# Performance work log

Measured on AMD Instinct MI355X. Metric: run time of the kernel, lower is better.

The kernel has to match this reference:

```python
import jax, jax.numpy as jnp
import numpy as np

K_NEIGHBORS = 16
BN_EPS = 1e-5


def _bn(h, g, b):
    # train-mode BatchNorm1d over (batch, points) per channel, biased variance
    mu = h.mean(axis=(0, 1))
    var = h.var(axis=(0, 1))
    return g * (h - mu) * jax.lax.rsqrt(var + BN_EPS) + b


def _gather(arr, idx):
    # arr: [B,N,D], idx: [B,N,K] -> [B,N,K,D]
    return jax.vmap(lambda a, i: a[i])(arr, idx)


def setup_inputs() -> dict:
    key = jax.random.key(0)
    ks = jax.random.split(key, 16)
    B, N, Cin, C, H, M = 4, 4096, 64, 64, 32, 4
    rn = lambda k, s: jax.random.normal(k, s, dtype=jnp.float32) * 0.05
    return {
        "x": jax.random.normal(ks[0], (B, N, Cin), dtype=jnp.float32),
        "p": jax.random.normal(ks[1], (B, N, 3), dtype=jnp.float32),
        "fc1_w": rn(ks[2], (Cin, C)), "fc1_b": jnp.zeros((C,), jnp.float32),
        "bn1_g": jnp.ones((C,), jnp.float32), "bn1_b": jnp.zeros((C,), jnp.float32),
        "qkv_w": rn(ks[3], (C, 3 * C)),
        "pos_w1": rn(ks[4], (3, H)), "pos_b1": jnp.zeros((H,), jnp.float32),
        "pos_w2": rn(ks[5], (H, C)), "pos_b2": jnp.zeros((C,), jnp.float32),
        "attn_w1": rn(ks[6], (C, M * C)), "attn_b1": jnp.zeros((M * C,), jnp.float32),
        "attn_w2": rn(ks[7], (M * C, C)), "attn_b2": jnp.zeros((C,), jnp.float32),
        "bn2_g": jnp.ones((C,), jnp.float32), "bn2_b": jnp.zeros((C,), jnp.float32),
        "fc2_w": rn(ks[8], (C, C)), "fc2_b": jnp.zeros((C,), jnp.float32),
        "bn3_g": jnp.ones((C,), jnp.float32), "bn3_b": jnp.zeros((C,), jnp.float32),
    }


def reference(x, p, fc1_w, fc1_b, bn1_g, bn1_b, qkv_w,
              pos_w1, pos_b1, pos_w2, pos_b2,
              attn_w1, attn_b1, attn_w2, attn_b2,
              bn2_g, bn2_b, fc2_w, fc2_b, bn3_g, bn3_b):
    C = fc1_w.shape[1]
    # fc1 -> BN -> ReLU
    h = jax.nn.relu(_bn(x @ fc1_w + fc1_b, bn1_g, bn1_b))
    residual = h

    # PointTransformerLayer (vector attention over kNN; mask is all-ones)
    qkv = h @ qkv_w  # [B,N,3C]
    q, k, v = qkv[..., :C], qkv[..., C:2 * C], qkv[..., 2 * C:]
    # squared pairwise distances (matches norm-based topk ranking)
    sq = jnp.sum(p * p, axis=-1)  # [B,N]
    d2 = sq[:, :, None] + sq[:, None, :] - 2.0 * jnp.einsum('bnd,bmd->bnm', p, p)
    _, idx = jax.lax.top_k(-d2, K_NEIGHBORS)  # k smallest distances, [B,N,K]

    kj = _gather(k, idx)          # [B,N,K,C]
    vj = _gather(v, idx)          # [B,N,K,C]
    pj = _gather(p, idx)          # [B,N,K,3]

    rel_pos = p[:, :, None, :] - pj                      # [B,N,K,3]
    pe = jax.nn.relu(rel_pos @ pos_w1 + pos_b1) @ pos_w2 + pos_b2  # [B,N,K,C]

    qk_rel = q[:, :, None, :] - kj                       # [B,N,K,C]
    vv = vj + pe
    sim = jax.nn.relu((qk_rel + pe) @ attn_w1 + attn_b1) @ attn_w2 + attn_b2
    attn = jax.nn.softmax(sim, axis=2)                   # softmax over neighbors
    agg = jnp.sum(attn * vv, axis=2)                     # [B,N,C]

    h2 = jax.nn.relu(_bn(agg, bn2_g, bn2_b))
    y = jax.nn.relu(_bn((h2 + residual) @ fc2_w + fc2_b, bn3_g, bn3_b))
    return (y, p)
```

## Files before the change

kernel.cpp:

```cpp
#include <hip/hip_runtime.h>
#include <math.h>

constexpr int kB = 4, kN = 4096, kK = 16;
constexpr int kRows = kB * kN;
constexpr float kEps = 1e-5f;
constexpr float kFltMax = 3.402823466e38f;
constexpr int kCap = 240;

typedef __attribute__((ext_vector_type(8))) short short8;
typedef __attribute__((ext_vector_type(4))) float f32x4;

__device__ __forceinline__ unsigned short f2bf(float x) {
  return (unsigned short)((__float_as_uint(x) + 0x8000u) >> 16);
}
__device__ __forceinline__ unsigned int pkbf(float lo, float hi) {
  return ((__float_as_uint(lo) + 0x8000u) >> 16) |
         ((__float_as_uint(hi) + 0x8000u) & 0xffff0000u);
}
__device__ __forceinline__ short8 pack8f(float4 a, float4 b) {
  union { unsigned int u[4]; short8 s; } pk;
  pk.u[0] = pkbf(a.x, a.y);
  pk.u[1] = pkbf(a.z, a.w);
  pk.u[2] = pkbf(b.x, b.y);
  pk.u[3] = pkbf(b.z, b.w);
  return pk.s;
}

__device__ __forceinline__ int lane_prefix(unsigned long long m) {
  return __builtin_amdgcn_mbcnt_hi((unsigned)(m >> 32),
         __builtin_amdgcn_mbcnt_lo((unsigned)m, 0));
}

__device__ __forceinline__ void bitonic64(float& sv, int& si, int lane) {
  #pragma unroll
  for (int k = 2; k <= 64; k <<= 1) {
    #pragma unroll
    for (int j = k >> 1; j > 0; j >>= 1) {
      float ov = __shfl_xor(sv, j);
      int   oi = __shfl_xor(si, j);
      bool up = ((lane & k) == 0);
      bool lower = ((lane & j) == 0);
      bool osm = (ov < sv) || (ov == sv && oi < si);
      bool take = (lower == up) ? osm : !osm;
      if (take) { sv = ov; si = oi; }
    }
  }
}

__global__ __launch_bounds__(256) void fc1_conv_kernel(
    const float* __restrict__ x, const float* __restrict__ w,
    const float* __restrict__ bias,
    const float* __restrict__ aw1, const float* __restrict__ aw2,
    const float* __restrict__ pw2, const float* __restrict__ qw,
    const float* __restrict__ f2w,
    const float* __restrict__ pin, float* __restrict__ p4o,
    unsigned short* __restrict__ wpak,
    float* __restrict__ out) {
  __shared__ unsigned short wf[8 * 512];
  const int t = threadIdx.x;
  const int blk = blockIdx.x;
  {
    int id = blk * 256 + t;
    if (id < 16384) {
      int j = id & 7, lane = (id >> 3) & 63, rest = id >> 9;
      int mt = rest >> 1, hh = rest & 1;
      wpak[id] = f2bf(aw1[(32 * hh + 8 * (lane >> 4) + j) * 256 + mt * 16 + (lane & 15)]);
      float3 pp = *reinterpret_cast<const float3*>(pin + 3 * id);
      float4 o;
      o.x = pp.x; o.y = pp.y; o.z = pp.z;
      o.w = pp.x * pp.x + pp.y * pp.y + pp.z * pp.z;
      *reinterpret_cast<float4*>(p4o + 4 * id) = o;
    } else if (id < 32768) {
      int i = id - 16384;
      int j = i & 7, lane = (i >> 3) & 63, rest = i >> 9;
      int ct = rest >> 3, f = rest & 7;
      wpak[id] = f2bf(aw2[(32 * f + 8 * (lane >> 4) + j) * 64 + ct * 16 + (lane & 15)]);
    } else if (id < 34816) {
      int i = id - 32768;
      int c = i >> 5, hh = i & 31;
      wpak[id] = f2bf(pw2[hh * 64 + c]);
    } else if (id < 47104) {
      int i = id - 34816;
      int j = i & 7, lane = (i >> 3) & 63, rest = i >> 9;
      int ct = rest >> 1, hh = rest & 1;
      wpak[id] = f2bf(qw[(32 * hh + 8 * (lane >> 4) + j) * 192 + ct * 16 + (lane & 15)]);
    } else if (id < 51200) {
      int i = id - 47104;
      int j = i & 7, lane = (i >> 3) & 63, rest = i >> 9;
      int ct = rest >> 1, hh = rest & 1;
      wpak[id] = f2bf(f2w[(32 * hh + 8 * (lane >> 4) + j) * 64 + ct * 16 + (lane & 15)]);
    }
  }
  for (int i = t; i < 4096; i += 256) {
    int j = i & 7, lane = (i >> 3) & 63, rest = i >> 9;
    int ct = rest >> 1, hh = rest & 1;
    wf[i] = f2bf(w[(32 * hh + 8 * (lane >> 4) + j) * 64 + ct * 16 + (lane & 15)]);
  }
  __syncthreads();
  const int lane = t & 63, wv = t >> 6;
  const int l = lane & 15, q = lane >> 4;
  const int r0 = blk * 64;
  const int row = r0 + wv * 16 + l;
  const f32x4 zero = {0.f, 0.f, 0.f, 0.f};
  float4 xa0 = *reinterpret_cast<const float4*>(&x[row * 64 + q * 8]);
  float4 xa1 = *reinterpret_cast<const float4*>(&x[row * 64 + q * 8 + 4]);
  float4 xb0 = *reinterpret_cast<const float4*>(&x[row * 64 + 32 + q * 8]);
  float4 xb1 = *reinterpret_cast<const float4*>(&x[row * 64 + 32 + q * 8 + 4]);
  short8 a0 = pack8f(xa0, xa1), a1 = pack8f(xb0, xb1);
  #pragma unroll
  for (int ct = 0; ct < 4; ++ct) {
    short8 b0 = *reinterpret_cast<const short8*>(&wf[(ct * 2 + 0) * 512 + lane * 8]);
    short8 b1 = *reinterpret_cast<const short8*>(&wf[(ct * 2 + 1) * 512 + lane * 8]);
    f32x4 acc = __builtin_amdgcn_mfma_f32_16x16x32_bf16(a0, b0, zero, 0, 0, 0);
    acc = __builtin_amdgcn_mfma_f32_16x16x32_bf16(a1, b1, acc, 0, 0, 0);
    const float bc = bias[ct * 16 + l];
    #pragma unroll
    for (int i = 0; i < 4; ++i)
      out[(r0 + wv * 16 + q * 4 + i) * 64 + ct * 16 + l] = acc[i] + bc;
  }
}

__global__ void stats_part_kernel(const float* __restrict__ src, float* __restrict__ part) {
  __shared__ float sb[256], sb2[256];
  const int t = threadIdx.x, blk = blockIdx.x;
  const int c = t & 63, rg = t >> 6;
  float s = 0.f, s2 = 0.f;
  for (int r = rg; r < 64; r += 4) {
    float v = src[(blk * 64 + r) * 64 + c];
    s += v; s2 += v * v;
  }
  sb[t] = s; sb2[t] = s2; __syncthreads();
  if (t < 64) {
    float ts  = sb[t] + sb[64 + t] + sb[128 + t] + sb[192 + t];
    float ts2 = sb2[t] + sb2[64 + t] + sb2[128 + t] + sb2[192 + t];
    part[blk * 128 + t] = ts;
    part[blk * 128 + 64 + t] = ts2;
  }
}

__global__ void stats_fin_kernel(const float* __restrict__ part,
                                 const float* __restrict__ g, const float* __restrict__ b,
                                 float* __restrict__ A, float* __restrict__ Bv) {
  const int c = threadIdx.x;
  double s = 0.0, s2 = 0.0;
  for (int i = 0; i < 256; ++i) { s += part[i * 128 + c]; s2 += part[i * 128 + 64 + c]; }
  double mean = s / (double)kRows;
  double var = s2 / (double)kRows - mean * mean;
  float rs = (float)(1.0 / sqrt(var + (double)kEps));
  float Af = g[c] * rs;
  A[c] = Af;
  Bv[c] = b[c] - (float)mean * Af;
}

__global__ __launch_bounds__(256) void qkv_bn_kernel(
    const float* __restrict__ hpre, const float* __restrict__ A1,
    const float* __restrict__ B1, const unsigned short* __restrict__ wqf,
    float* __restrict__ hout, unsigned short* __restrict__ out) {
  const int t = threadIdx.x, lane = t & 63, wv = t >> 6;
  const int l = lane & 15, q = lane >> 4;
  const int r0 = blockIdx.x * 64;
  const int row = r0 + wv * 16 + l;
  const f32x4 zero = {0.f, 0.f, 0.f, 0.f};
  short8 af[2];
  #pragma unroll
  for (int hh = 0; hh < 2; ++hh) {
    const int c0 = 32 * hh + q * 8;
    float4 v0 = *reinterpret_cast<const float4*>(&hpre[row * 64 + c0]);
    float4 v1 = *reinterpret_cast<const float4*>(&hpre[row * 64 + c0 + 4]);
    float4 Aa = *reinterpret_cast<const float4*>(&A1[c0]);
    float4 Ab = *reinterpret_cast<const float4*>(&A1[c0 + 4]);
    float4 Ba = *reinterpret_cast<const float4*>(&B1[c0]);
    float4 Bb = *reinterpret_cast<const float4*>(&B1[c0 + 4]);
    v0.x = fmaxf(Aa.x * v0.x + Ba.x, 0.f); v0.y = fmaxf(Aa.y * v0.y + Ba.y, 0.f);
    v0.z = fmaxf(Aa.z * v0.z + Ba.z, 0.f); v0.w = fmaxf(Aa.w * v0.w + Ba.w, 0.f);
    v1.x = fmaxf(Ab.x * v1.x + Bb.x, 0.f); v1.y = fmaxf(Ab.y * v1.y + Bb.y, 0.f);
    v1.z = fmaxf(Ab.z * v1.z + Bb.z, 0.f); v1.w = fmaxf(Ab.w * v1.w + Bb.w, 0.f);
    *reinterpret_cast<float4*>(&hout[row * 64 + c0]) = v0;
    *reinterpret_cast<float4*>(&hout[row * 64 + c0 + 4]) = v1;
    af[hh] = pack8f(v0, v1);
  }
  #pragma unroll
  for (int ct = 0; ct < 12; ++ct) {
    short8 b0 = *reinterpret_cast<const short8*>(&wqf[((ct * 2 + 0) * 64 + lane) * 8]);
    short8 b1 = *reinterpret_cast<const short8*>(&wqf[((ct * 2 + 1) * 64 + lane) * 8]);
    f32x4 acc = __builtin_amdgcn_mfma_f32_16x16x32_bf16(af[0], b0, zero, 0, 0, 0);
    acc = __builtin_amdgcn_mfma_f32_16x16x32_bf16(af[1], b1, acc, 0, 0, 0);
    #pragma unroll
    for (int i = 0; i < 4; ++i)
      out[(r0 + wv * 16 + q * 4 + i) * 192 + ct * 16 + l] = f2bf(acc[i]);
  }
}

__global__ __launch_bounds__(256) void knn_attn_kernel(
    const float* __restrict__ p4, const unsigned short* __restrict__ qkv,
    const float* __restrict__ pos_w1, const float* __restrict__ pos_b1,
    const float* __restrict__ pos_b2,
    const float* __restrict__ attn_b1, const float* __restrict__ attn_b2,
    const unsigned short* __restrict__ w1f,
    const unsigned short* __restrict__ w2f,
    const unsigned short* __restrict__ pw2t,
    float* __restrict__ agg) {
  __shared__ unsigned short Ulds[64 * 72];
  __shared__ float VVlds[64 * 68];
  __shared__ int   scnt[4];
  __shared__ float sthr[4];

  const int t = threadIdx.x;
  const int lane = t & 63, w = t >> 6;
  const int l = lane & 15, q = lane >> 4;
  const int work = ((blockIdx.x & 7) << 9) | (blockIdx.x >> 3);
  const int b = work >> 10;
  const int pt_row = work * 4 + w;
  const int qrow0 = work * 4;
  const int base = b * kN;
  const f32x4 zero = {0.f, 0.f, 0.f, 0.f};

  if (t < 4) scnt[t] = 0;

  const float4 q0f = *reinterpret_cast<const float4*>(p4 + 4 * (qrow0 + 0));
  const float4 q1f = *reinterpret_cast<const float4*>(p4 + 4 * (qrow0 + 1));
  const float4 q2f = *reinterpret_cast<const float4*>(p4 + 4 * (qrow0 + 2));
  const float4 q3f = *reinterpret_cast<const float4*>(p4 + 4 * (qrow0 + 3));
  const float4 qp4 = *reinterpret_cast<const float4*>(p4 + 4 * pt_row);
  const float qx = qp4.x, qy = qp4.y, qz = qp4.z, sqq = qp4.w;

  auto d2q = [](const float4& Q, const float4& C) -> float {
    float dt = fmaf(Q.z, C.z, fmaf(Q.y, C.y, Q.x * C.x));
    return fmaf(-2.0f, dt, Q.w + C.w);
  };
  unsigned pk0[8], pk1[8], pk2[8], pk3[8];
  float lmin = kFltMax;
  const int cbase = base + w * 1024;
  #pragma unroll
  for (int g = 0; g < 2; ++g) {
    float4 cc[8];
    #pragma unroll
    for (int jj = 0; jj < 8; ++jj)
      cc[jj] = *reinterpret_cast<const float4*>(p4 + 4 * (cbase + (g * 8 + jj) * 64 + lane));
    #pragma unroll
    for (int jj = 0; jj < 8; ++jj) {
      float dot = fmaf(qz, cc[jj].z, fmaf(qy, cc[jj].y, qx * cc[jj].x));
      lmin = fminf(lmin, fmaf(-2.0f, dot, sqq + cc[jj].w));
    }
    #pragma unroll
    for (int pi = 0; pi < 4; ++pi) {
      const float4 ca = cc[2 * pi], cb = cc[2 * pi + 1];
      pk0[g * 4 + pi] = (__float_as_uint(d2q(q0f, ca)) >> 16) |
                        (__float_as_uint(d2q(q0f, cb)) & 0xffff0000u);
      pk1[g * 4 + pi] = (__float_as_uint(d2q(q1f, ca)) >> 16) |
                        (__float_as_uint(d2q(q1f, cb)) & 0xffff0000u);
      pk2[g * 4 + pi] = (__float_as_uint(d2q(q2f, ca)) >> 16) |
                        (__float_as_uint(d2q(q2f, cb)) & 0xffff0000u);
      pk3[g * 4 + pi] = (__float_as_uint(d2q(q3f, ca)) >> 16) |
                        (__float_as_uint(d2q(q3f, cb)) & 0xffff0000u);
    }
  }
  {
    int dummy = lane;
    float lm = lmin;
    bitonic64(lm, dummy, lane);
    float s16 = __shfl(lm, 15);
    if (lane == 0) sthr[w] = s16 + 1e-3f;
  }
  __syncthreads();

  {
    auto append_q = [&](const unsigned (&PK)[8], int j) {
      int* listj = reinterpret_cast<int*>(VVlds + j * 1088);
      const float thrj = sthr[j];
      #pragma unroll
      for (int g = 0; g < 2; ++g) {
        unsigned long long m[8];
        int pc[8];
        #pragma unroll
        for (int c = 0; c < 8; ++c) {
          unsigned pku = PK[g * 4 + (c >> 1)];
          float dv = (c & 1) ? __uint_as_float(pku & 0xffff0000u)
                             : __uint_as_float(pku << 16);
          m[c] = __ballot(dv <= thrj);
          pc[c] = __popcll(m[c]);
        }
        int tot = pc[0] + pc[1] + pc[2] + pc[3] + pc[4] + pc[5] + pc[6] + pc[7];
        int old = 0;
        if (lane == 0) old = atomicAdd(&scnt[j], tot);
        old = __shfl(old, 0);
        int pre = 0;
        #pragma unroll
        for (int c = 0; c < 8; ++c) {
          if ((m[c] >> lane) & 1ull) {
            int pos = old + pre + lane_prefix(m[c]);
            if (pos < kCap) listj[pos] = w * 1024 + (g * 8 + c) * 64 + lane;
          }
          pre += pc[c];
        }
      }
    };
    append_q(pk0, 0);
    append_q(pk1, 1);
    append_q(pk2, 2);
    append_q(pk3, 3);
  }
  __syncthreads();

  const int n = scnt[w];
  int* bufi = reinterpret_cast<int*>(VVlds + w * 1088);
  float sv = kFltMax;
  int   si = 0x7fffffff;
  if (n <= kCap) {
    for (int g0 = 0; g0 < n; g0 += 48) {
      float mv; int mi;
      if (lane < 16) { mv = sv; mi = si; }
      else {
        int pos = g0 + (lane - 16);
        if (pos < n) {
          int jj = bufi[pos];
          float4 c = *reinterpret_cast<const float4*>(p4 + 4 * (base + jj));
          float dot = fmaf(qz, c.z, fmaf(qy, c.y, qx * c.x));
          mv = fmaf(-2.0f, dot, sqq + c.w);
          mi = jj;
        } else { mv = kFltMax; mi = 0x7fffffff; }
      }
      bitonic64(mv, mi, lane);
      sv = mv; si = mi;
    }
  } else {
    for (int g0 = 0; g0 < kN; g0 += 48) {
      float mv; int mi;
      if (lane < 16) { mv = sv; mi = si; }
      else {
        int j = g0 + (lane - 16);
        if (j < kN) {
          float4 c = *reinterpret_cast<const float4*>(p4 + 4 * (base + j));
          float dot = fmaf(qz, c.z, fmaf(qy, c.y, qx * c.x));
          mv = fmaf(-2.0f, dot, sqq + c.w);
          mi = j;
        } else { mv = kFltMax; mi = 0x7fffffff; }
      }
      bitonic64(mv, mi, lane);
      sv = mv; si = mi;
    }
  }

  int idxv = 0;
  if (lane < 16) {
    int o = si;
    if ((unsigned)o >= (unsigned)kN) o = 0;
    idxv = o;
  }

  asm volatile("" ::: "memory");

  {
    const int r = lane >> 2, seg = lane & 3;
    const unsigned short* jrow = qkv + (base + __shfl(idxv, r)) * 192;
    const int c0 = seg * 16;
    uint4 k0 = *reinterpret_cast<const uint4*>(jrow + 64 + c0);
    uint4 k1 = *reinterpret_cast<const uint4*>(jrow + 64 + c0 + 8);
    uint4 v0 = *reinterpret_cast<const uint4*>(jrow + 128 + c0);
    uint4 v1 = *reinterpret_cast<const uint4*>(jrow + 128 + c0 + 8);
    uint4 q0 = *reinterpret_cast<const uint4*>(qkv + pt_row * 192 + c0);
    uint4 q1 = *reinterpret_cast<const uint4*>(qkv + pt_row * 192 + c0 + 8);
    auto diff2 = [](unsigned int qu, unsigned int ku) -> unsigned int {
      float lo = __uint_as_float(qu << 16) - __uint_as_float(ku << 16);
      float hi = __uint_as_float(qu & 0xffff0000u) - __uint_as_float(ku & 0xffff0000u);
      return pkbf(lo, hi);
    };
    uint4 u0, u1;
    u0.x = diff2(q0.x, k0.x); u0.y = diff2(q0.y, k0.y);
    u0.z = diff2(q0.z, k0.z); u0.w = diff2(q0.w, k0.w);
    u1.x = diff2(q1.x, k1.x); u1.y = diff2(q1.y, k1.y);
    u1.z = diff2(q1.z, k1.z); u1.w = diff2(q1.w, k1.w);
    *reinterpret_cast<uint4*>(&Ulds[(w * 16 + r) * 72 + c0]) = u0;
    *reinterpret_cast<uint4*>(&Ulds[(w * 16 + r) * 72 + c0 + 8]) = u1;
    const unsigned int vs[8] = {v0.x, v0.y, v0.z, v0.w, v1.x, v1.y, v1.z, v1.w};
    #pragma unroll
    for (int i = 0; i < 4; ++i) {
      float4 vv;
      vv.x = __uint_as_float(vs[2 * i] << 16);
      vv.y = __uint_as_float(vs[2 * i] & 0xffff0000u);
      vv.z = __uint_as_float(vs[2 * i + 1] << 16);
      vv.w = __uint_as_float(vs[2 * i + 1] & 0xffff0000u);
      *reinterpret_cast<float4*>(&VVlds[(w * 16 + r) * 68 + c0 + 4 * i]) = vv;
    }
  }
  short8 pbf;
  {
    const int nj = __shfl(idxv, l);
    const float4 pj4 = *reinterpret_cast<const float4*>(p4 + 4 * (base + nj));
    float rx = qx - pj4.x, ry = qy - pj4.y, rz = qz - pj4.z;
    float hv[8];
    #pragma unroll
    for (int j = 0; j < 8; ++j) {
      int hh = q * 8 + j;
      hv[j] = fmaxf(pos_b1[hh] + rx * pos_w1[hh] + ry * pos_w1[32 + hh] +
                    rz * pos_w1[64 + hh], 0.0f);
    }
    union { unsigned int u[4]; short8 s; } pk;
    #pragma unroll
    for (int ii = 0; ii < 4; ++ii) pk.u[ii] = pkbf(hv[2 * ii], hv[2 * ii + 1]);
    pbf = pk.s;
  }

  {
    const int urow = (w * 16 + l) * 72;
    const int vrow = (w * 16 + l) * 68;
    #pragma unroll
    for (int mt = 0; mt < 4; ++mt) {
      short8 paf = *reinterpret_cast<const short8*>(&pw2t[(mt * 16 + l) * 32 + q * 8]);
      f32x4 pe = __builtin_amdgcn_mfma_f32_16x16x32_bf16(paf, pbf, zero, 0, 0, 0);
      const int c0 = mt * 16 + q * 4;
      float4 b2v = *reinterpret_cast<const float4*>(&pos_b2[c0]);
      float pe0 = pe[0] + b2v.x, pe1 = pe[1] + b2v.y;
      float pe2 = pe[2] + b2v.z, pe3 = pe[3] + b2v.w;
      uint2 u2 = *reinterpret_cast<uint2*>(&Ulds[urow + c0]);
      uint2 o;
      o.x = pkbf(__uint_as_float(u2.x << 16) + pe0,
                 __uint_as_float(u2.x & 0xffff0000u) + pe1);
      o.y = pkbf(__uint_as_float(u2.y << 16) + pe2,
                 __uint_as_float(u2.y & 0xffff0000u) + pe3);
      *reinterpret_cast<uint2*>(&Ulds[urow + c0]) = o;
      float4 vv = *reinterpret_cast<float4*>(&VVlds[vrow + c0]);
      vv.x += pe0; vv.y += pe1; vv.z += pe2; vv.w += pe3;
      *reinterpret_cast<float4*>(&VVlds[vrow + c0]) = vv;
    }
  }

  unsigned int plo[16], phi[16];
  {
    const int urow = (w * 16 + l) * 72;
    short8 ub0 = *reinterpret_cast<const short8*>(&Ulds[urow + q * 8]);
    short8 ub1 = *reinterpret_cast<const short8*>(&Ulds[urow + 32 + q * 8]);
    #pragma unroll
    for (int mt = 0; mt < 16; ++mt) {
      short8 a0 = *reinterpret_cast<const short8*>(&w1f[(mt * 2 + 0) * 512 + lane * 8]);
      short8 a1 = *reinterpret_cast<const short8*>(&w1f[(mt * 2 + 1) * 512 + lane * 8]);
      f32x4 acc = __builtin_amdgcn_mfma_f32_16x16x32_bf16(a0, ub0, zero, 0, 0, 0);
      acc = __builtin_amdgcn_mfma_f32_16x16x32_bf16(a1, ub1, acc, 0, 0, 0);
      float4 bb = *reinterpret_cast<const float4*>(&attn_b1[mt * 16 + q * 4]);
      plo[mt] = pkbf(fmaxf(acc[0] + bb.x, 0.f), fmaxf(acc[1] + bb.y, 0.f));
      phi[mt] = pkbf(fmaxf(acc[2] + bb.z, 0.f), fmaxf(acc[3] + bb.w, 0.f));
    }
  }

  {
    f32x4 acc2[4];
    #pragma unroll
    for (int ct = 0; ct < 4; ++ct) acc2[ct] = zero;
    const int sbase = l + 32 * (q & 1);
    const bool hi_mt = (q >= 2);
    #pragma unroll
    for (int f = 0; f < 8; ++f) {
      union { unsigned int u[4]; short8 s; } pk;
      #pragma unroll
      for (int d = 0; d < 4; ++d) {
        const int src = sbase + ((d >> 1) << 4);
        const unsigned int w0 = (d & 1) ? phi[2 * f] : plo[2 * f];
        const unsigned int w1v = (d & 1) ? phi[2 * f + 1] : plo[2 * f + 1];
        unsigned int va = (unsigned int)__shfl((int)w0, src);
        unsigned int vb = (unsigned int)__shfl((int)w1v, src);
        pk.u[d] = hi_mt ? vb : va;
      }
      short8 afr = pk.s;
      #pragma unroll
      for (int ct = 0; ct < 4; ++ct) {
        short8 bfr = *reinterpret_cast<const short8*>(&w2f[((ct * 8 + f) * 64 + lane) * 8]);
        acc2[ct] = __builtin_amdgcn_mfma_f32_16x16x32_bf16(afr, bfr, acc2[ct], 0, 0, 0);
      }
    }
    #pragma unroll
    for (int ct = 0; ct < 4; ++ct) {
      const int ch = ct * 16 + l;
      const float bv = attn_b2[ch];
      float s0v = acc2[ct][0] + bv, s1v = acc2[ct][1] + bv;
      float s2v = acc2[ct][2] + bv, s3v = acc2[ct][3] + bv;
      float mx = fmaxf(fmaxf(s0v, s1v), fmaxf(s2v, s3v));
      mx = fmaxf(mx, __shfl_xor(mx, 16, 64));
      mx = fmaxf(mx, __shfl_xor(mx, 32, 64));
      float e0 = __expf(s0v - mx), e1 = __expf(s1v - mx);
      float e2 = __expf(s2v - mx), e3 = __expf(s3v - mx);
      float se = e0 + e1 + e2 + e3;
      se += __shfl_xor(se, 16, 64);
      se += __shfl_xor(se, 32, 64);
      const int vbase = (w * 16 + q * 4) * 68 + ch;
      float a = e0 * VVlds[vbase] + e1 * VVlds[vbase + 68] +
                e2 * VVlds[vbase + 136] + e3 * VVlds[vbase + 204];
      a += __shfl_xor(a, 16, 64);
      a += __shfl_xor(a, 32, 64);
      if (q == 0) agg[pt_row * 64 + ch] = a / se;
    }
  }
}

__global__ __launch_bounds__(256) void fc2_mfma_kernel(
    const float* __restrict__ aggp, const float* __restrict__ hres,
    const float* __restrict__ A2, const float* __restrict__ B2,
    const unsigned short* __restrict__ fc2f, const float* __restrict__ bias,
    float* __restrict__ z) {
  const int t = threadIdx.x, lane = t & 63, wv = t >> 6;
  const int l = lane & 15, q = lane >> 4;
  const int r0 = blockIdx.x * 64;
  const int row = r0 + wv * 16 + l;
  const f32x4 zero = {0.f, 0.f, 0.f, 0.f};
  short8 af[2];
  #pragma unroll
  for (int hh = 0; hh < 2; ++hh) {
    const int c0 = 32 * hh + q * 8;
    float4 v0 = *reinterpret_cast<const float4*>(&aggp[row * 64 + c0]);
    float4 v1 = *reinterpret_cast<const float4*>(&aggp[row * 64 + c0 + 4]);
    float4 r0v = *reinterpret_cast<const float4*>(&hres[row * 64 + c0]);
    float4 r1v = *reinterpret_cast<const float4*>(&hres[row * 64 + c0 + 4]);
    float4 Aa = *reinterpret_cast<const float4*>(&A2[c0]);
    float4 Ab = *reinterpret_cast<const float4*>(&A2[c0 + 4]);
    float4 Ba = *reinterpret_cast<const float4*>(&B2[c0]);
    float4 Bb = *reinterpret_cast<const float4*>(&B2[c0 + 4]);
    v0.x = fmaxf(Aa.x * v0.x + Ba.x, 0.f) + r0v.x;
    v0.y = fmaxf(Aa.y * v0.y + Ba.y, 0.f) + r0v.y;
    v0.z = fmaxf(Aa.z * v0.z + Ba.z, 0.f) + r0v.z;
    v0.w = fmaxf(Aa.w * v0.w + Ba.w, 0.f) + r0v.w;
    v1.x = fmaxf(Ab.x * v1.x + Bb.x, 0.f) + r1v.x;
    v1.y = fmaxf(Ab.y * v1.y + Bb.y, 0.f) + r1v.y;
    v1.z = fmaxf(Ab.z * v1.z + Bb.z, 0.f) + r1v.z;
    v1.w = fmaxf(Ab.w * v1.w + Bb.w, 0.f) + r1v.w;
    af[hh] = pack8f(v0, v1);
  }
  #pragma unroll
  for (int ct = 0; ct < 4; ++ct) {
    short8 b0 = *reinterpret_cast<const short8*>(&fc2f[((ct * 2 + 0) * 64 + lane) * 8]);
    short8 b1 = *reinterpret_cast<const short8*>(&fc2f[((ct * 2 + 1) * 64 + lane) * 8]);
    f32x4 acc = __builtin_amdgcn_mfma_f32_16x16x32_bf16(af[0], b0, zero, 0, 0, 0);
    acc = __builtin_amdgcn_mfma_f32_16x16x32_bf16(af[1], b1, acc, 0, 0, 0);
    const float bc = bias[ct * 16 + l];
    #pragma unroll
    for (int i = 0; i < 4; ++i)
      z[(r0 + wv * 16 + q * 4 + i) * 64 + ct * 16 + l] = acc[i] + bc;
  }
}

__global__ void final_kernel(const float* __restrict__ z, const float* __restrict__ A3,
                             const float* __restrict__ B3, const float* __restrict__ p,
                             float* __restrict__ y) {
  const int blk = blockIdx.x, t = threadIdx.x;
  if (blk < 4096) {
    int i = blk * 256 + t;
    int c = i & 63;
    y[i] = fmaxf(A3[c] * z[i] + B3[c], 0.0f);
  } else {
    int i = (blk - 4096) * 256 + t;
    y[1048576 + i] = p[i];
  }
}

extern "C" void kernel_launch(void* const* d_in, const int* in_sizes, int n_in,
                              void* d_out, int out_size, void* d_ws, size_t ws_size,
                              hipStream_t stream) {
  const float* x       = (const float*)d_in[0];
  const float* p       = (const float*)d_in[1];
  const float* fc1_w   = (const float*)d_in[2];
  const float* fc1_b   = (const float*)d_in[3];
  const float* bn1_g   = (const float*)d_in[4];
  const float* bn1_b   = (const float*)d_in[5];
  const float* qkv_w   = (const float*)d_in[6];
  const float* pos_w1  = (const float*)d_in[7];
  const float* pos_b1  = (const float*)d_in[8];
  const float* pos_w2  = (const float*)d_in[9];
  const float* pos_b2  = (const float*)d_in[10];
  const float* attn_w1 = (const float*)d_in[11];
  const float* attn_b1 = (const float*)d_in[12];
  const float* attn_w2 = (const float*)d_in[13];
  const float* attn_b2 = (const float*)d_in[14];
  const float* bn2_g   = (const float*)d_in[15];
  const float* bn2_b   = (const float*)d_in[16];
  const float* fc2_w   = (const float*)d_in[17];
  const float* fc2_b   = (const float*)d_in[18];
  const float* bn3_g   = (const float*)d_in[19];
  const float* bn3_b   = (const float*)d_in[20];

  float* ws   = (float*)d_ws;
  float* h    = ws;
  unsigned short* qkvb = (unsigned short*)(ws + 1048576);
  float* hpre = ws + 4194304;
  float* aggv = ws + 5242880;
  float* z    = ws + 6291456;
  float* st   = ws + 7340032;
  float* p4   = ws + 7356800;
  unsigned short* wpak = (unsigned short*)(ws + 7618944);
  unsigned short* w1f  = wpak;
  unsigned short* w2f  = wpak + 16384;
  unsigned short* pw2t = wpak + 32768;
  unsigned short* wqf  = wpak + 34816;
  unsigned short* fc2f = wpak + 47104;

  float* A1 = st,       *B1 = st + 64;
  float* A2 = st + 128, *B2 = st + 192;
  float* A3 = st + 256, *B3 = st + 320;
  float* y = (float*)d_out;

  fc1_conv_kernel<<<256, 256, 0, stream>>>(x, fc1_w, fc1_b, attn_w1, attn_w2,
                                           pos_w2, qkv_w, fc2_w, p, p4, wpak, hpre);
  stats_part_kernel<<<256, 256, 0, stream>>>(hpre, aggv);
  stats_fin_kernel<<<1, 64, 0, stream>>>(aggv, bn1_g, bn1_b, A1, B1);
  qkv_bn_kernel<<<256, 256, 0, stream>>>(hpre, A1, B1, wqf, h, qkvb);
  knn_attn_kernel<<<4096, 256, 0, stream>>>(p4, qkvb, pos_w1, pos_b1, pos_b2,
                                            attn_b1, attn_b2, w1f, w2f, pw2t, aggv);
  stats_part_kernel<<<256, 256, 0, stream>>>(aggv, z);
  stats_fin_kernel<<<1, 64, 0, stream>>>(z, bn2_g, bn2_b, A2, B2);
  fc2_mfma_kernel<<<256, 256, 0, stream>>>(aggv, h, A2, B2, fc2f, fc2_b, z);
  stats_part_kernel<<<256, 256, 0, stream>>>(z, aggv);
  stats_fin_kernel<<<1, 64, 0, stream>>>(aggv, bn3_g, bn3_b, A3, B3);
  final_kernel<<<4288, 256, 0, stream>>>(z, A3, B3, p, y);
}
```

Before: 288.4 us.

## Tighten kNN candidate threshold across waves, store VV in bf16, interleave MLP layers

```diff
diff --git a/kernel.cpp b/kernel.cpp
--- a/kernel.cpp
+++ b/kernel.cpp
@@ -16,6 +16,11 @@
 __device__ __forceinline__ unsigned int pkbf(float lo, float hi) {
   return ((__float_as_uint(lo) + 0x8000u) >> 16) |
          ((__float_as_uint(hi) + 0x8000u) & 0xffff0000u);
+}
+__device__ __forceinline__ float bflo(unsigned int u) { return __uint_as_float(u << 16); }
+__device__ __forceinline__ float bfhi(unsigned int u) { return __uint_as_float(u & 0xffff0000u); }
+__device__ __forceinline__ float bfu16(unsigned short us) {
+  return __uint_as_float(((unsigned int)us) << 16);
 }
 __device__ __forceinline__ short8 pack8f(float4 a, float4 b) {
   union { unsigned int u[4]; short8 s; } pk;
@@ -45,6 +50,11 @@
       if (take) { sv = ov; si = oi; }
     }
   }
+}
+
+__device__ __forceinline__ float d2q(const float4& Q, const float4& C) {
+  float dt = fmaf(Q.z, C.z, fmaf(Q.y, C.y, Q.x * C.x));
+  return fmaf(-2.0f, dt, Q.w + C.w);
 }
 
 __global__ __launch_bounds__(256) void fc1_conv_kernel(
@@ -201,9 +211,9 @@
     const unsigned short* __restrict__ pw2t,
     float* __restrict__ agg) {
   __shared__ unsigned short Ulds[64 * 72];
-  __shared__ float VVlds[64 * 68];
-  __shared__ int   scnt[4];
-  __shared__ float sthr[4];
+  __shared__ unsigned short VVb[64 * 72];
+  __shared__ float thrs[4];
+  __shared__ int   cnts[4];
 
   const int t = threadIdx.x;
   const int lane = t & 63, w = t >> 6;
@@ -215,21 +225,18 @@
   const int base = b * kN;
   const f32x4 zero = {0.f, 0.f, 0.f, 0.f};
 
-  if (t < 4) scnt[t] = 0;
-
-  const float4 q0f = *reinterpret_cast<const float4*>(p4 + 4 * (qrow0 + 0));
-  const float4 q1f = *reinterpret_cast<const float4*>(p4 + 4 * (qrow0 + 1));
-  const float4 q2f = *reinterpret_cast<const float4*>(p4 + 4 * (qrow0 + 2));
-  const float4 q3f = *reinterpret_cast<const float4*>(p4 + 4 * (qrow0 + 3));
-  const float4 qp4 = *reinterpret_cast<const float4*>(p4 + 4 * pt_row);
-  const float qx = qp4.x, qy = qp4.y, qz = qp4.z, sqq = qp4.w;
-
-  auto d2q = [](const float4& Q, const float4& C) -> float {
-    float dt = fmaf(Q.z, C.z, fmaf(Q.y, C.y, Q.x * C.x));
-    return fmaf(-2.0f, dt, Q.w + C.w);
-  };
-  unsigned pk0[8], pk1[8], pk2[8], pk3[8];
-  float lmin = kFltMax;
+  if (t < 4) cnts[t] = 0;
+
+  float4 qs[4];
+  qs[0] = *reinterpret_cast<const float4*>(p4 + 4 * (qrow0 + 0));
+  qs[1] = *reinterpret_cast<const float4*>(p4 + 4 * (qrow0 + 1));
+  qs[2] = *reinterpret_cast<const float4*>(p4 + 4 * (qrow0 + 2));
+  qs[3] = *reinterpret_cast<const float4*>(p4 + 4 * (qrow0 + 3));
+  const float4 qp4 = (w == 0) ? qs[0] : (w == 1) ? qs[1] : (w == 2) ? qs[2] : qs[3];
+  const float qx = qp4.x, qy = qp4.y, qz = qp4.z;
+
+  unsigned pks[4][8];
+  float lm[4] = {kFltMax, kFltMax, kFltMax, kFltMax};
   const int cbase = base + w * 1024;
   #pragma unroll
   for (int g = 0; g < 2; ++g) {
@@ -238,36 +245,40 @@
     for (int jj = 0; jj < 8; ++jj)
       cc[jj] = *reinterpret_cast<const float4*>(p4 + 4 * (cbase + (g * 8 + jj) * 64 + lane));
     #pragma unroll
-    for (int jj = 0; jj < 8; ++jj) {
-      float dot = fmaf(qz, cc[jj].z, fmaf(qy, cc[jj].y, qx * cc[jj].x));
-      lmin = fminf(lmin, fmaf(-2.0f, dot, sqq + cc[jj].w));
-    }
-    #pragma unroll
     for (int pi = 0; pi < 4; ++pi) {
       const float4 ca = cc[2 * pi], cb = cc[2 * pi + 1];
-      pk0[g * 4 + pi] = (__float_as_uint(d2q(q0f, ca)) >> 16) |
-                        (__float_as_uint(d2q(q0f, cb)) & 0xffff0000u);
-      pk1[g * 4 + pi] = (__float_as_uint(d2q(q1f, ca)) >> 16) |
-                        (__float_as_uint(d2q(q1f, cb)) & 0xffff0000u);
-      pk2[g * 4 + pi] = (__float_as_uint(d2q(q2f, ca)) >> 16) |
-                        (__float_as_uint(d2q(q2f, cb)) & 0xffff0000u);
-      pk3[g * 4 + pi] = (__float_as_uint(d2q(q3f, ca)) >> 16) |
-                        (__float_as_uint(d2q(q3f, cb)) & 0xffff0000u);
-    }
-  }
-  {
+      #pragma unroll
+      for (int j = 0; j < 4; ++j) {
+        float da = d2q(qs[j], ca);
+        float db = d2q(qs[j], cb);
+        lm[j] = fminf(lm[j], fminf(da, db));
+        pks[j][g * 4 + pi] = (__float_as_uint(da) >> 16) |
+                             (__float_as_uint(db) & 0xffff0000u);
+      }
+    }
+  }
+  {
+    float* lmbuf = reinterpret_cast<float*>(Ulds);
+    #pragma unroll
+    for (int j = 0; j < 4; ++j) lmbuf[w * 256 + j * 64 + lane] = lm[j];
+  }
+  __syncthreads();
+
+  {
+    const float* lmbuf = reinterpret_cast<const float*>(Ulds);
+    float cv = fminf(fminf(lmbuf[w * 64 + lane], lmbuf[256 + w * 64 + lane]),
+                     fminf(lmbuf[512 + w * 64 + lane], lmbuf[768 + w * 64 + lane]));
     int dummy = lane;
-    float lm = lmin;
-    bitonic64(lm, dummy, lane);
-    float s16 = __shfl(lm, 15);
-    if (lane == 0) sthr[w] = s16 + 1e-3f;
+    bitonic64(cv, dummy, lane);
+    float s16 = __shfl(cv, 15);
+    if (lane == 0) thrs[w] = s16 + fabsf(s16) * 0.0078125f + 1e-6f;
   }
   __syncthreads();
 
   {
     auto append_q = [&](const unsigned (&PK)[8], int j) {
-      int* listj = reinterpret_cast<int*>(VVlds + j * 1088);
-      const float thrj = sthr[j];
+      int* listj = reinterpret_cast<int*>(VVb + j * 1152);
+      const float thrj = thrs[j];
       #pragma unroll
       for (int g = 0; g < 2; ++g) {
         unsigned long long m[8];
@@ -282,7 +293,7 @@
         }
         int tot = pc[0] + pc[1] + pc[2] + pc[3] + pc[4] + pc[5] + pc[6] + pc[7];
         int old = 0;
-        if (lane == 0) old = atomicAdd(&scnt[j], tot);
+        if (lane == 0) old = atomicAdd(&cnts[j], tot);
         old = __shfl(old, 0);
         int pre = 0;
         #pragma unroll
@@ -295,15 +306,15 @@
         }
       }
     };
-    append_q(pk0, 0);
-    append_q(pk1, 1);
-    append_q(pk2, 2);
-    append_q(pk3, 3);
+    append_q(pks[0], 0);
+    append_q(pks[1], 1);
+    append_q(pks[2], 2);
+    append_q(pks[3], 3);
   }
   __syncthreads();
 
-  const int n = scnt[w];
-  int* bufi = reinterpret_cast<int*>(VVlds + w * 1088);
+  const int n = cnts[w];
+  const int* bufi = reinterpret_cast<const int*>(VVb + w * 1152);
   float sv = kFltMax;
   int   si = 0x7fffffff;
   if (n <= kCap) {
@@ -315,8 +326,7 @@
         if (pos < n) {
           int jj = bufi[pos];
           float4 c = *reinterpret_cast<const float4*>(p4 + 4 * (base + jj));
-          float dot = fmaf(qz, c.z, fmaf(qy, c.y, qx * c.x));
-          mv = fmaf(-2.0f, dot, sqq + c.w);
+          mv = d2q(qp4, c);
           mi = jj;
         } else { mv = kFltMax; mi = 0x7fffffff; }
       }
@@ -331,8 +341,7 @@
         int j = g0 + (lane - 16);
         if (j < kN) {
           float4 c = *reinterpret_cast<const float4*>(p4 + 4 * (base + j));
-          float dot = fmaf(qz, c.z, fmaf(qy, c.y, qx * c.x));
-          mv = fmaf(-2.0f, dot, sqq + c.w);
+          mv = d2q(qp4, c);
           mi = j;
         } else { mv = kFltMax; mi = 0x7fffffff; }
       }
@@ -361,8 +370,8 @@
     uint4 q0 = *reinterpret_cast<const uint4*>(qkv + pt_row * 192 + c0);
     uint4 q1 = *reinterpret_cast<const uint4*>(qkv + pt_row * 192 + c0 + 8);
     auto diff2 = [](unsigned int qu, unsigned int ku) -> unsigned int {
-      float lo = __uint_as_float(qu << 16) - __uint_as_float(ku << 16);
-      float hi = __uint_as_float(qu & 0xffff0000u) - __uint_as_float(ku & 0xffff0000u);
+      float lo = bflo(qu) - bflo(ku);
+      float hi = bfhi(qu) - bfhi(ku);
       return pkbf(lo, hi);
     };
     uint4 u0, u1;
@@ -372,16 +381,8 @@
     u1.z = diff2(q1.z, k1.z); u1.w = diff2(q1.w, k1.w);
     *reinterpret_cast<uint4*>(&Ulds[(w * 16 + r) * 72 + c0]) = u0;
     *reinterpret_cast<uint4*>(&Ulds[(w * 16 + r) * 72 + c0 + 8]) = u1;
-    const unsigned int vs[8] = {v0.x, v0.y, v0.z, v0.w, v1.x, v1.y, v1.z, v1.w};
-    #pragma unroll
-    for (int i = 0; i < 4; ++i) {
-      float4 vv;
-      vv.x = __uint_as_float(vs[2 * i] << 16);
-      vv.y = __uint_as_float(vs[2 * i] & 0xffff0000u);
-      vv.z = __uint_as_float(vs[2 * i + 1] << 16);
-      vv.w = __uint_as_float(vs[2 * i + 1] & 0xffff0000u);
-      *reinterpret_cast<float4*>(&VVlds[(w * 16 + r) * 68 + c0 + 4 * i]) = vv;
-    }
+    *reinterpret_cast<uint4*>(&VVb[(w * 16 + r) * 72 + c0]) = v0;
+    *reinterpret_cast<uint4*>(&VVb[(w * 16 + r) * 72 + c0 + 8]) = v1;
   }
   short8 pbf;
   {
@@ -403,7 +404,6 @@
 
   {
     const int urow = (w * 16 + l) * 72;
-    const int vrow = (w * 16 + l) * 68;
     #pragma unroll
     for (int mt = 0; mt < 4; ++mt) {
       short8 paf = *reinterpret_cast<const short8*>(&pw2t[(mt * 16 + l) * 32 + q * 8]);
@@ -414,48 +414,46 @@
       float pe2 = pe[2] + b2v.z, pe3 = pe[3] + b2v.w;
       uint2 u2 = *reinterpret_cast<uint2*>(&Ulds[urow + c0]);
       uint2 o;
-      o.x = pkbf(__uint_as_float(u2.x << 16) + pe0,
-                 __uint_as_float(u2.x & 0xffff0000u) + pe1);
-      o.y = pkbf(__uint_as_float(u2.y << 16) + pe2,
-                 __uint_as_float(u2.y & 0xffff0000u) + pe3);
+      o.x = pkbf(bflo(u2.x) + pe0, bfhi(u2.x) + pe1);
+      o.y = pkbf(bflo(u2.y) + pe2, bfhi(u2.y) + pe3);
       *reinterpret_cast<uint2*>(&Ulds[urow + c0]) = o;
-      float4 vv = *reinterpret_cast<float4*>(&VVlds[vrow + c0]);
-      vv.x += pe0; vv.y += pe1; vv.z += pe2; vv.w += pe3;
-      *reinterpret_cast<float4*>(&VVlds[vrow + c0]) = vv;
-    }
-  }
-
-  unsigned int plo[16], phi[16];
-  {
+      uint2 v2 = *reinterpret_cast<uint2*>(&VVb[urow + c0]);
+      uint2 ov;
+      ov.x = pkbf(bflo(v2.x) + pe0, bfhi(v2.x) + pe1);
+      ov.y = pkbf(bflo(v2.y) + pe2, bfhi(v2.y) + pe3);
+      *reinterpret_cast<uint2*>(&VVb[urow + c0]) = ov;
+    }
+  }
+
+  {
+    f32x4 acc2[4];
+    #pragma unroll
+    for (int ct = 0; ct < 4; ++ct) acc2[ct] = zero;
     const int urow = (w * 16 + l) * 72;
     short8 ub0 = *reinterpret_cast<const short8*>(&Ulds[urow + q * 8]);
     short8 ub1 = *reinterpret_cast<const short8*>(&Ulds[urow + 32 + q * 8]);
-    #pragma unroll
-    for (int mt = 0; mt < 16; ++mt) {
-      short8 a0 = *reinterpret_cast<const short8*>(&w1f[(mt * 2 + 0) * 512 + lane * 8]);
-      short8 a1 = *reinterpret_cast<const short8*>(&w1f[(mt * 2 + 1) * 512 + lane * 8]);
-      f32x4 acc = __builtin_amdgcn_mfma_f32_16x16x32_bf16(a0, ub0, zero, 0, 0, 0);
-      acc = __builtin_amdgcn_mfma_f32_16x16x32_bf16(a1, ub1, acc, 0, 0, 0);
-      float4 bb = *reinterpret_cast<const float4*>(&attn_b1[mt * 16 + q * 4]);
-      plo[mt] = pkbf(fmaxf(acc[0] + bb.x, 0.f), fmaxf(acc[1] + bb.y, 0.f));
-      phi[mt] = pkbf(fmaxf(acc[2] + bb.z, 0.f), fmaxf(acc[3] + bb.w, 0.f));
-    }
-  }
-
-  {
-    f32x4 acc2[4];
-    #pragma unroll
-    for (int ct = 0; ct < 4; ++ct) acc2[ct] = zero;
     const int sbase = l + 32 * (q & 1);
     const bool hi_mt = (q >= 2);
     #pragma unroll
     for (int f = 0; f < 8; ++f) {
+      unsigned plo2[2], phi2[2];
+      #pragma unroll
+      for (int s = 0; s < 2; ++s) {
+        const int mt = 2 * f + s;
+        short8 a0 = *reinterpret_cast<const short8*>(&w1f[(mt * 2 + 0) * 512 + lane * 8]);
+        short8 a1 = *reinterpret_cast<const short8*>(&w1f[(mt * 2 + 1) * 512 + lane * 8]);
+        f32x4 acc = __builtin_amdgcn_mfma_f32_16x16x32_bf16(a0, ub0, zero, 0, 0, 0);
+        acc = __builtin_amdgcn_mfma_f32_16x16x32_bf16(a1, ub1, acc, 0, 0, 0);
+        float4 bb = *reinterpret_cast<const float4*>(&attn_b1[mt * 16 + q * 4]);
+        plo2[s] = pkbf(fmaxf(acc[0] + bb.x, 0.f), fmaxf(acc[1] + bb.y, 0.f));
+        phi2[s] = pkbf(fmaxf(acc[2] + bb.z, 0.f), fmaxf(acc[3] + bb.w, 0.f));
+      }
       union { unsigned int u[4]; short8 s; } pk;
       #pragma unroll
       for (int d = 0; d < 4; ++d) {
         const int src = sbase + ((d >> 1) << 4);
-        const unsigned int w0 = (d & 1) ? phi[2 * f] : plo[2 * f];
-        const unsigned int w1v = (d & 1) ? phi[2 * f + 1] : plo[2 * f + 1];
+        const unsigned int w0 = (d & 1) ? phi2[0] : plo2[0];
+        const unsigned int w1v = (d & 1) ? phi2[1] : plo2[1];
         unsigned int va = (unsigned int)__shfl((int)w0, src);
         unsigned int vb = (unsigned int)__shfl((int)w1v, src);
         pk.u[d] = hi_mt ? vb : va;
@@ -481,9 +479,9 @@
       float se = e0 + e1 + e2 + e3;
       se += __shfl_xor(se, 16, 64);
       se += __shfl_xor(se, 32, 64);
-      const int vbase = (w * 16 + q * 4) * 68 + ch;
-      float a = e0 * VVlds[vbase] + e1 * VVlds[vbase + 68] +
-                e2 * VVlds[vbase + 136] + e3 * VVlds[vbase + 204];
+      const int vbase = (w * 16 + q * 4) * 72 + ch;
+      float a = e0 * bfu16(VVb[vbase])       + e1 * bfu16(VVb[vbase + 72]) +
+                e2 * bfu16(VVb[vbase + 144]) + e3 * bfu16(VVb[vbase + 216]);
       a += __shfl_xor(a, 16, 64);
       a += __shfl_xor(a, 32, 64);
       if (q == 0) agg[pt_row * 64 + ch] = a / se;
```

Result: slower. 309.5 us (+7.3%).

## Store V+pe in bf16 LDS, interleave attn MLP layers, raise occupancy

Applied to the files above, without the earlier changes.

```diff
diff --git a/kernel.cpp b/kernel.cpp
--- a/kernel.cpp
+++ b/kernel.cpp
@@ -16,6 +16,11 @@
 __device__ __forceinline__ unsigned int pkbf(float lo, float hi) {
   return ((__float_as_uint(lo) + 0x8000u) >> 16) |
          ((__float_as_uint(hi) + 0x8000u) & 0xffff0000u);
+}
+__device__ __forceinline__ float bflo(unsigned int u) { return __uint_as_float(u << 16); }
+__device__ __forceinline__ float bfhi(unsigned int u) { return __uint_as_float(u & 0xffff0000u); }
+__device__ __forceinline__ float bfu16(unsigned short us) {
+  return __uint_as_float(((unsigned int)us) << 16);
 }
 __device__ __forceinline__ short8 pack8f(float4 a, float4 b) {
   union { unsigned int u[4]; short8 s; } pk;
@@ -45,6 +50,11 @@
       if (take) { sv = ov; si = oi; }
     }
   }
+}
+
+__device__ __forceinline__ float d2q(const float4& Q, const float4& C) {
+  float dt = fmaf(Q.z, C.z, fmaf(Q.y, C.y, Q.x * C.x));
+  return fmaf(-2.0f, dt, Q.w + C.w);
 }
 
 __global__ __launch_bounds__(256) void fc1_conv_kernel(
@@ -191,7 +201,7 @@
   }
 }
 
-__global__ __launch_bounds__(256) void knn_attn_kernel(
+__global__ __launch_bounds__(256, 4) void knn_attn_kernel(
     const float* __restrict__ p4, const unsigned short* __restrict__ qkv,
     const float* __restrict__ pos_w1, const float* __restrict__ pos_b1,
     const float* __restrict__ pos_b2,
@@ -201,9 +211,9 @@
     const unsigned short* __restrict__ pw2t,
     float* __restrict__ agg) {
   __shared__ unsigned short Ulds[64 * 72];
-  __shared__ float VVlds[64 * 68];
+  __shared__ unsigned short VVb[64 * 72];
+  __shared__ float sthr[4];
   __shared__ int   scnt[4];
-  __shared__ float sthr[4];
 
   const int t = threadIdx.x;
   const int lane = t & 63, w = t >> 6;
@@ -224,10 +234,6 @@
   const float4 qp4 = *reinterpret_cast<const float4*>(p4 + 4 * pt_row);
   const float qx = qp4.x, qy = qp4.y, qz = qp4.z, sqq = qp4.w;
 
-  auto d2q = [](const float4& Q, const float4& C) -> float {
-    float dt = fmaf(Q.z, C.z, fmaf(Q.y, C.y, Q.x * C.x));
-    return fmaf(-2.0f, dt, Q.w + C.w);
-  };
   unsigned pk0[8], pk1[8], pk2[8], pk3[8];
   float lmin = kFltMax;
   const int cbase = base + w * 1024;
@@ -266,7 +272,7 @@
 
   {
     auto append_q = [&](const unsigned (&PK)[8], int j) {
-      int* listj = reinterpret_cast<int*>(VVlds + j * 1088);
+      int* listj = reinterpret_cast<int*>(VVb) + j * 576;
       const float thrj = sthr[j];
       #pragma unroll
       for (int g = 0; g < 2; ++g) {
@@ -303,7 +309,7 @@
   __syncthreads();
 
   const int n = scnt[w];
-  int* bufi = reinterpret_cast<int*>(VVlds + w * 1088);
+  const int* bufi = reinterpret_cast<const int*>(VVb) + w * 576;
   float sv = kFltMax;
   int   si = 0x7fffffff;
   if (n <= kCap) {
@@ -315,8 +321,7 @@
         if (pos < n) {
           int jj = bufi[pos];
           float4 c = *reinterpret_cast<const float4*>(p4 + 4 * (base + jj));
-          float dot = fmaf(qz, c.z, fmaf(qy, c.y, qx * c.x));
-          mv = fmaf(-2.0f, dot, sqq + c.w);
+          mv = d2q(qp4, c);
           mi = jj;
         } else { mv = kFltMax; mi = 0x7fffffff; }
       }
@@ -331,8 +336,7 @@
         int j = g0 + (lane - 16);
         if (j < kN) {
           float4 c = *reinterpret_cast<const float4*>(p4 + 4 * (base + j));
-          float dot = fmaf(qz, c.z, fmaf(qy, c.y, qx * c.x));
-          mv = fmaf(-2.0f, dot, sqq + c.w);
+          mv = d2q(qp4, c);
           mi = j;
         } else { mv = kFltMax; mi = 0x7fffffff; }
       }
@@ -361,8 +365,8 @@
     uint4 q0 = *reinterpret_cast<const uint4*>(qkv + pt_row * 192 + c0);
     uint4 q1 = *reinterpret_cast<const uint4*>(qkv + pt_row * 192 + c0 + 8);
     auto diff2 = [](unsigned int qu, unsigned int ku) -> unsigned int {
-      float lo = __uint_as_float(qu << 16) - __uint_as_float(ku << 16);
-      float hi = __uint_as_float(qu & 0xffff0000u) - __uint_as_float(ku & 0xffff0000u);
+      float lo = bflo(qu) - bflo(ku);
+      float hi = bfhi(qu) - bfhi(ku);
       return pkbf(lo, hi);
     };
     uint4 u0, u1;
@@ -372,16 +376,8 @@
     u1.z = diff2(q1.z, k1.z); u1.w = diff2(q1.w, k1.w);
     *reinterpret_cast<uint4*>(&Ulds[(w * 16 + r) * 72 + c0]) = u0;
     *reinterpret_cast<uint4*>(&Ulds[(w * 16 + r) * 72 + c0 + 8]) = u1;
-    const unsigned int vs[8] = {v0.x, v0.y, v0.z, v0.w, v1.x, v1.y, v1.z, v1.w};
-    #pragma unroll
-    for (int i = 0; i < 4; ++i) {
-      float4 vv;
-      vv.x = __uint_as_float(vs[2 * i] << 16);
-      vv.y = __uint_as_float(vs[2 * i] & 0xffff0000u);
-      vv.z = __uint_as_float(vs[2 * i + 1] << 16);
-      vv.w = __uint_as_float(vs[2 * i + 1] & 0xffff0000u);
-      *reinterpret_cast<float4*>(&VVlds[(w * 16 + r) * 68 + c0 + 4 * i]) = vv;
-    }
+    *reinterpret_cast<uint4*>(&VVb[(w * 16 + r) * 72 + c0]) = v0;
+    *reinterpret_cast<uint4*>(&VVb[(w * 16 + r) * 72 + c0 + 8]) = v1;
   }
   short8 pbf;
   {
@@ -403,7 +399,6 @@
 
   {
     const int urow = (w * 16 + l) * 72;
-    const int vrow = (w * 16 + l) * 68;
     #pragma unroll
     for (int mt = 0; mt < 4; ++mt) {
       short8 paf = *reinterpret_cast<const short8*>(&pw2t[(mt * 16 + l) * 32 + q * 8]);
@@ -414,48 +409,46 @@
       float pe2 = pe[2] + b2v.z, pe3 = pe[3] + b2v.w;
       uint2 u2 = *reinterpret_cast<uint2*>(&Ulds[urow + c0]);
       uint2 o;
-      o.x = pkbf(__uint_as_float(u2.x << 16) + pe0,
-                 __uint_as_float(u2.x & 0xffff0000u) + pe1);
-      o.y = pkbf(__uint_as_float(u2.y << 16) + pe2,
-                 __uint_as_float(u2.y & 0xffff0000u) + pe3);
+      o.x = pkbf(bflo(u2.x) + pe0, bfhi(u2.x) + pe1);
+      o.y = pkbf(bflo(u2.y) + pe2, bfhi(u2.y) + pe3);
       *reinterpret_cast<uint2*>(&Ulds[urow + c0]) = o;
-      float4 vv = *reinterpret_cast<float4*>(&VVlds[vrow + c0]);
-      vv.x += pe0; vv.y += pe1; vv.z += pe2; vv.w += pe3;
-      *reinterpret_cast<float4*>(&VVlds[vrow + c0]) = vv;
-    }
-  }
-
-  unsigned int plo[16], phi[16];
+      uint2 v2 = *reinterpret_cast<uint2*>(&VVb[urow + c0]);
+      uint2 ov;
+      ov.x = pkbf(bflo(v2.x) + pe0, bfhi(v2.x) + pe1);
+      ov.y = pkbf(bflo(v2.y) + pe2, bfhi(v2.y) + pe3);
+      *reinterpret_cast<uint2*>(&VVb[urow + c0]) = ov;
+    }
+  }
+
   {
+    f32x4 acc2[4];
+    #pragma unroll
+    for (int ct = 0; ct < 4; ++ct) acc2[ct] = zero;
     const int urow = (w * 16 + l) * 72;
     short8 ub0 = *reinterpret_cast<const short8*>(&Ulds[urow + q * 8]);
     short8 ub1 = *reinterpret_cast<const short8*>(&Ulds[urow + 32 + q * 8]);
-    #pragma unroll
-    for (int mt = 0; mt < 16; ++mt) {
-      short8 a0 = *reinterpret_cast<const short8*>(&w1f[(mt * 2 + 0) * 512 + lane * 8]);
-      short8 a1 = *reinterpret_cast<const short8*>(&w1f[(mt * 2 + 1) * 512 + lane * 8]);
-      f32x4 acc = __builtin_amdgcn_mfma_f32_16x16x32_bf16(a0, ub0, zero, 0, 0, 0);
-      acc = __builtin_amdgcn_mfma_f32_16x16x32_bf16(a1, ub1, acc, 0, 0, 0);
-      float4 bb = *reinterpret_cast<const float4*>(&attn_b1[mt * 16 + q * 4]);
-      plo[mt] = pkbf(fmaxf(acc[0] + bb.x, 0.f), fmaxf(acc[1] + bb.y, 0.f));
-      phi[mt] = pkbf(fmaxf(acc[2] + bb.z, 0.f), fmaxf(acc[3] + bb.w, 0.f));
-    }
-  }
-
-  {
-    f32x4 acc2[4];
-    #pragma unroll
-    for (int ct = 0; ct < 4; ++ct) acc2[ct] = zero;
     const int sbase = l + 32 * (q & 1);
     const bool hi_mt = (q >= 2);
     #pragma unroll
     for (int f = 0; f < 8; ++f) {
+      unsigned plo2[2], phi2[2];
+      #pragma unroll
+      for (int s = 0; s < 2; ++s) {
+        const int mt = 2 * f + s;
+        short8 a0 = *reinterpret_cast<const short8*>(&w1f[(mt * 2 + 0) * 512 + lane * 8]);
+        short8 a1 = *reinterpret_cast<const short8*>(&w1f[(mt * 2 + 1) * 512 + lane * 8]);
+        f32x4 acc = __builtin_amdgcn_mfma_f32_16x16x32_bf16(a0, ub0, zero, 0, 0, 0);
+        acc = __builtin_amdgcn_mfma_f32_16x16x32_bf16(a1, ub1, acc, 0, 0, 0);
+        float4 bb = *reinterpret_cast<const float4*>(&attn_b1[mt * 16 + q * 4]);
+        plo2[s] = pkbf(fmaxf(acc[0] + bb.x, 0.f), fmaxf(acc[1] + bb.y, 0.f));
+        phi2[s] = pkbf(fmaxf(acc[2] + bb.z, 0.f), fmaxf(acc[3] + bb.w, 0.f));
+      }
       union { unsigned int u[4]; short8 s; } pk;
       #pragma unroll
       for (int d = 0; d < 4; ++d) {
         const int src = sbase + ((d >> 1) << 4);
-        const unsigned int w0 = (d & 1) ? phi[2 * f] : plo[2 * f];
-        const unsigned int w1v = (d & 1) ? phi[2 * f + 1] : plo[2 * f + 1];
+        const unsigned int w0 = (d & 1) ? phi2[0] : plo2[0];
+        const unsigned int w1v = (d & 1) ? phi2[1] : plo2[1];
         unsigned int va = (unsigned int)__shfl((int)w0, src);
         unsigned int vb = (unsigned int)__shfl((int)w1v, src);
         pk.u[d] = hi_mt ? vb : va;
@@ -481,9 +474,9 @@
       float se = e0 + e1 + e2 + e3;
       se += __shfl_xor(se, 16, 64);
       se += __shfl_xor(se, 32, 64);
-      const int vbase = (w * 16 + q * 4) * 68 + ch;
-      float a = e0 * VVlds[vbase] + e1 * VVlds[vbase + 68] +
-                e2 * VVlds[vbase + 136] + e3 * VVlds[vbase + 204];
+      const int vbase = (w * 16 + q * 4) * 72 + ch;
+      float a = e0 * bfu16(VVb[vbase])       + e1 * bfu16(VVb[vbase + 72]) +
+                e2 * bfu16(VVb[vbase + 144]) + e3 * bfu16(VVb[vbase + 216]);
       a += __shfl_xor(a, 16, 64);
       a += __shfl_xor(a, 32, 64);
       if (q == 0) agg[pt_row * 64 + ch] = a / se;
```

Measured after the change: 268.0 us. 7.0% less time.
